# Kernel tuning notes

Hardware: AMD Instinct MI355X
Metric: run time of the kernel (lower is better)

## Reference

```python
import jax, jax.numpy as jnp
import numpy as np

EPS = 1e-12  # torch F.normalize default eps


def setup_inputs() -> dict:
    key = jax.random.key(0)
    k1, k2, k3, k4 = jax.random.split(key, 4)
    B, M, D = 4, 8192, 512
    N, P = 128, 1
    x = jax.random.normal(k1, (B, M, D), dtype=jnp.float32)
    phi = jax.random.normal(k2, (D, N, P), dtype=jnp.float32) * (1.0 / D ** 0.5)
    scale = jnp.ones((1,), dtype=jnp.float32)
    W = jax.random.normal(k3, (N, D, D), dtype=jnp.float32) * (1.0 / D ** 0.5)
    b = jax.random.normal(k4, (N, D), dtype=jnp.float32) * 0.01
    return {"x": x, "phi": phi, "scale": scale, "W": W, "b": b}


def _l2norm(v, axis):
    return v / jnp.maximum(jnp.linalg.norm(v, axis=axis, keepdims=True), EPS)


def reference(x, phi, scale, W, b):
    # normalize tokens along feature dim, phi along dim axis, scale phi
    xn = _l2norm(x, axis=2)                      # [B,M,D]
    phin = scale * _l2norm(phi, axis=0)          # [D,N,P]
    logits = jnp.einsum('bmd,dnp->bmnp', xn, phin)
    B, M, N, P = logits.shape
    d = jax.nn.softmax(logits, axis=1)           # dispatch weights (over tokens)
    c = jax.nn.softmax(logits.reshape(B, M, N * P), axis=-1).reshape(B, M, N, P)  # combine (over slots)
    xs = jnp.einsum('bmd,bmnp->bnpd', xn, d)     # slot inputs [B,N,P,D]
    # per-expert Linear, batched over experts (grouped GEMM)
    ys = jnp.einsum('bnpd,nde->bnpe', xs, W) + b[None, :, None, :]
    y = jnp.einsum('bnpd,bmnp->bmd', ys, c)
    return y
```

## Files before the change

kernel.cpp:

```cpp
#include <hip/hip_runtime.h>
#include <math.h>

#define B_ 4
#define M_ 8192
#define D_ 512
#define N_ 128
#define TOK (B_ * M_)
#define MC_ 16
#define MLEN (M_ / MC_)

#define OFF_CS 0
#define OFF_XS (OFF_CS + 512)
#define OFF_PBT (OFF_XS + B_ * N_ * D_)
#define OFF_E (OFF_PBT + N_ * D_ / 2)
#define OFF_EWT (OFF_E + (size_t)TOK * N_)
#define OFF_XBT (OFF_EWT + (size_t)N_ * TOK / 2)
#define OFF_YST (OFF_XBT + (size_t)D_ * TOK / 2)
#define OFF_XP (OFF_YST + B_ * D_ * N_ / 2)

typedef __attribute__((ext_vector_type(8))) short s16x8;
typedef __attribute__((ext_vector_type(4))) float f32x4;

__device__ inline short f2bf(float f) {
    union { float f; unsigned u; } v;
    v.f = f;
    unsigned r = v.u + 0x7fffu + ((v.u >> 16) & 1u);
    return (short)(r >> 16);
}

__global__ __launch_bounds__(128) void k_phinorm(const float* __restrict__ phi,
                                                 const float* __restrict__ scale,
                                                 short* __restrict__ pbt) {
    __shared__ float sred[128];
    int n = blockIdx.x, tid = threadIdx.x;
    float ss = 0.f;
    for (int d = tid; d < D_; d += 128) {
        float v = phi[d * N_ + n];
        ss += v * v;
    }
    sred[tid] = ss;
    __syncthreads();
    for (int s = 64; s > 0; s >>= 1) {
        if (tid < s) sred[tid] += sred[tid + s];
        __syncthreads();
    }
    float sc = scale[0] / fmaxf(sqrtf(sred[0]), 1e-12f);
    for (int d = tid; d < D_; d += 128) pbt[n * D_ + d] = f2bf(phi[d * N_ + n] * sc);
}

__global__ __launch_bounds__(512) void k_logits(const float* __restrict__ x,
                                                const short* __restrict__ pbt,
                                                float* __restrict__ E,
                                                short* __restrict__ ewt,
                                                short* __restrict__ xbt,
                                                float* __restrict__ colsum) {
    __shared__ short smem[2 * 128 * 40];
    __shared__ float rnS[128];
    short* As = smem;
    short* Bs = smem + 128 * 40;
    int t = threadIdx.x;
    int r0 = blockIdx.x * 128;
    int sm = t >> 2;
    int kq = (t & 3) * 8;
    const float* xrow = &x[(size_t)(r0 + sm) * D_ + kq];
    const short* brow = &pbt[sm * D_ + kq];
    int wid = t >> 6, lane = t & 63;
    int quad = lane >> 4, l15 = lane & 15;
    int mw = (wid >> 1) * 32, nw = (wid & 1) * 64;
    int dl = t & 31, mg = t >> 5;
    f32x4 acc[2][4] = {};
    float ss = 0.f;

    for (int k0 = 0; k0 < D_; k0 += 32) {
        float4 a0 = *(const float4*)&xrow[k0];
        float4 a1 = *(const float4*)&xrow[k0 + 4];
        ss += a0.x * a0.x + a0.y * a0.y + a0.z * a0.z + a0.w * a0.w +
              a1.x * a1.x + a1.y * a1.y + a1.z * a1.z + a1.w * a1.w;
        s16x8 av;
        av[0] = f2bf(a0.x); av[1] = f2bf(a0.y); av[2] = f2bf(a0.z); av[3] = f2bf(a0.w);
        av[4] = f2bf(a1.x); av[5] = f2bf(a1.y); av[6] = f2bf(a1.z); av[7] = f2bf(a1.w);
        s16x8 bv = *(const s16x8*)&brow[k0];
        *(s16x8*)&As[sm * 40 + kq] = av;
        *(s16x8*)&Bs[sm * 40 + kq] = bv;
        __syncthreads();
        s16x8 af[2], bf[4];
#pragma unroll
        for (int i = 0; i < 2; i++)
            af[i] = *(const s16x8*)&As[(mw + i * 16 + l15) * 40 + quad * 8];
#pragma unroll
        for (int j = 0; j < 4; j++)
            bf[j] = *(const s16x8*)&Bs[(nw + j * 16 + l15) * 40 + quad * 8];
#pragma unroll
        for (int i = 0; i < 2; i++)
#pragma unroll
            for (int j = 0; j < 4; j++)
                acc[i][j] = __builtin_amdgcn_mfma_f32_16x16x32_bf16(af[i], bf[j], acc[i][j], 0, 0, 0);
        {
            s16x8 tv;
#pragma unroll
            for (int r = 0; r < 8; r++) tv[r] = As[(mg * 8 + r) * 40 + dl];
            *(s16x8*)&xbt[(size_t)(k0 + dl) * TOK + r0 + mg * 8] = tv;
        }
        __syncthreads();
    }
    ss += __shfl_xor(ss, 1, 64);
    ss += __shfl_xor(ss, 2, 64);
    if ((t & 3) == 0) rnS[sm] = 1.0f / fmaxf(sqrtf(ss), 1e-12f);
    __syncthreads();

    int bb = r0 >> 13;
    float rv[2][4];
#pragma unroll
    for (int i = 0; i < 2; i++) {
        int ml = mw + i * 16 + quad * 4;
        rv[i][0] = rnS[ml]; rv[i][1] = rnS[ml + 1];
        rv[i][2] = rnS[ml + 2]; rv[i][3] = rnS[ml + 3];
    }
    short4 ebf[2][4];
#pragma unroll
    for (int j = 0; j < 4; j++) {
        int n = nw + j * 16 + l15;
        float cs = 0.f;
#pragma unroll
        for (int i = 0; i < 2; i++) {
            int mb = r0 + mw + i * 16 + quad * 4;
            f32x4 vv = acc[i][j];
            float e0 = __expf(vv[0] * rv[i][0]), e1 = __expf(vv[1] * rv[i][1]);
            float e2 = __expf(vv[2] * rv[i][2]), e3 = __expf(vv[3] * rv[i][3]);
            cs += e0 + e1 + e2 + e3;
            E[(size_t)(mb + 0) * N_ + n] = e0;
            E[(size_t)(mb + 1) * N_ + n] = e1;
            E[(size_t)(mb + 2) * N_ + n] = e2;
            E[(size_t)(mb + 3) * N_ + n] = e3;
            short4 eb = {f2bf(e0 * rv[i][0]), f2bf(e1 * rv[i][1]),
                         f2bf(e2 * rv[i][2]), f2bf(e3 * rv[i][3])};
            ebf[i][j] = eb;
        }
        cs += __shfl_xor(cs, 16, 64);
        cs += __shfl_xor(cs, 32, 64);
        if (lane < 16) atomicAdd(&colsum[bb * N_ + n], cs);
    }
    short* T = smem;
#pragma unroll
    for (int h = 0; h < 2; h++) {
        if ((wid & 1) == h) {
#pragma unroll
            for (int i = 0; i < 2; i++) {
                int mb = mw + i * 16 + quad * 4;
#pragma unroll
                for (int j = 0; j < 4; j++) {
                    int nl = j * 16 + l15;
                    *(short4*)&T[nl * 136 + mb] = ebf[i][j];
                }
            }
        }
        __syncthreads();
        {
            int nl = t >> 3, c = t & 7;
            s16x8 v0 = *(const s16x8*)&T[nl * 136 + c * 16];
            s16x8 v1 = *(const s16x8*)&T[nl * 136 + c * 16 + 8];
            size_t go = (size_t)(h * 64 + nl) * TOK + r0 + c * 16;
            *(s16x8*)&ewt[go] = v0;
            *(s16x8*)&ewt[go + 8] = v1;
        }
        __syncthreads();
    }
}

__global__ __launch_bounds__(256) void k_xs(const short* __restrict__ ewt,
                                            const short* __restrict__ xbt,
                                            float* __restrict__ part) {
    __shared__ short An[128 * 40];
    __shared__ short Bd[128 * 40];
    int t = threadIdx.x;
    int bid = blockIdx.x;
    int bi = (bid & 7) * 32 + (bid >> 3);
    int dt = bi & 3, mc = (bi >> 2) & 15, b = bi >> 6;
    int d0 = dt * 128;
    size_t mbase = (size_t)b * M_ + (size_t)mc * MLEN;
    int srow = t >> 1, shalf = (t & 1) * 16;
    const short* arow = &ewt[(size_t)srow * TOK + mbase + shalf];
    const short* brow = &xbt[(size_t)(d0 + srow) * TOK + mbase + shalf];
    int wid = t >> 6, lane = t & 63;
    int quad = lane >> 4, l15 = lane & 15;
    int nw = (wid >> 1) * 64, dw = (wid & 1) * 64;
    f32x4 acc[4][4] = {};

    for (int k0 = 0; k0 < MLEN; k0 += 32) {
        s16x8 a0 = *(const s16x8*)&arow[k0];
        s16x8 a1 = *(const s16x8*)&arow[k0 + 8];
        s16x8 b0 = *(const s16x8*)&brow[k0];
        s16x8 b1 = *(const s16x8*)&brow[k0 + 8];
        *(s16x8*)&An[srow * 40 + shalf] = a0;
        *(s16x8*)&An[srow * 40 + shalf + 8] = a1;
        *(s16x8*)&Bd[srow * 40 + shalf] = b0;
        *(s16x8*)&Bd[srow * 40 + shalf + 8] = b1;
        __syncthreads();
        s16x8 af[4], bf[4];
#pragma unroll
        for (int i = 0; i < 4; i++)
            af[i] = *(const s16x8*)&An[(nw + i * 16 + l15) * 40 + quad * 8];
#pragma unroll
        for (int j = 0; j < 4; j++)
            bf[j] = *(const s16x8*)&Bd[(dw + j * 16 + l15) * 40 + quad * 8];
#pragma unroll
        for (int i = 0; i < 4; i++)
#pragma unroll
            for (int j = 0; j < 4; j++)
                acc[i][j] = __builtin_amdgcn_mfma_f32_16x16x32_bf16(af[i], bf[j], acc[i][j], 0, 0, 0);
        __syncthreads();
    }
    size_t pbase = (((size_t)mc * B_ + b) * N_) * D_ + d0;
#pragma unroll
    for (int i = 0; i < 4; i++) {
        int nb = nw + i * 16 + quad * 4;
#pragma unroll
        for (int j = 0; j < 4; j++) {
            int d = dw + j * 16 + l15;
            f32x4 vv = acc[i][j];
            part[pbase + (size_t)(nb + 0) * D_ + d] = vv[0];
            part[pbase + (size_t)(nb + 1) * D_ + d] = vv[1];
            part[pbase + (size_t)(nb + 2) * D_ + d] = vv[2];
            part[pbase + (size_t)(nb + 3) * D_ + d] = vv[3];
        }
    }
}

__global__ __launch_bounds__(256) void k_xsum(const float* __restrict__ part,
                                              const float* __restrict__ colsum,
                                              float* __restrict__ xs) {
    int bi = blockIdx.x;
    int tid = threadIdx.x;
    float inv = 1.0f / colsum[bi];
    size_t base = (size_t)bi * D_ + tid * 2;
    float sx = 0.f, sy = 0.f;
#pragma unroll 8
    for (int mc = 0; mc < MC_; mc++) {
        float2 v = *(const float2*)&part[(size_t)mc * (B_ * N_ * D_) + base];
        sx += v.x;
        sy += v.y;
    }
    float2 o = {sx * inv, sy * inv};
    *(float2*)&xs[base] = o;
}

__global__ __launch_bounds__(256) void k_ys(const float* __restrict__ xs,
                                            const float* __restrict__ W,
                                            const float* __restrict__ bias,
                                            short* __restrict__ ysT) {
    __shared__ float xsn[B_][D_];
    int bi = blockIdx.x;
    int n = bi >> 2, eq = bi & 3;
    int tid = threadIdx.x;
    {
        int lb = tid >> 6, ld = (tid & 63) * 4;
        *(float4*)&xsn[lb][ld] = *(const float4*)&xs[((size_t)lb * N_ + n) * D_ + ld];
        *(float4*)&xsn[lb][256 + ld] =
            *(const float4*)&xs[((size_t)lb * N_ + n) * D_ + 256 + ld];
    }
    __syncthreads();
    int b = tid >> 6;
    int e = eq * 128 + (tid & 63) * 2;
    const float* Wn = W + (size_t)n * D_ * D_ + e;
    float a0 = 0.f, a1 = 0.f;
#pragma unroll 8
    for (int d = 0; d < D_; d++) {
        float2 w = *(const float2*)&Wn[(size_t)d * D_];
        float xv = xsn[b][d];
        a0 += xv * w.x;
        a1 += xv * w.y;
    }
    float2 bv = *(const float2*)&bias[n * D_ + e];
    ysT[((size_t)b * D_ + e) * N_ + n] = f2bf(a0 + bv.x);
    ysT[((size_t)b * D_ + e + 1) * N_ + n] = f2bf(a1 + bv.y);
}

__global__ __launch_bounds__(256) void k_combine(const float* __restrict__ E,
                                                 const short* __restrict__ ysT,
                                                 float* __restrict__ y) {
    __shared__ short As[128 * 40];
    __shared__ short Bs[128 * 40];
    __shared__ float rsA[2][128];
    __shared__ float rsinv[128];
    int t = threadIdx.x;
    int bid = blockIdx.x;
    int bi = (bid & 7) * 128 + (bid >> 3);
    int dt = bi & 3, mt = bi >> 2;
    int r0 = mt * 128, d0 = dt * 128;
    int bb = r0 >> 13;
    int sm = t >> 1, nh = (t & 1) * 16;
    const float* erow = &E[(size_t)(r0 + sm) * N_ + nh];
    const short* yrow = &ysT[((size_t)bb * D_ + d0 + sm) * N_ + nh];
    int wid = t >> 6, lane = t & 63;
    int quad = lane >> 4, l15 = lane & 15;
    int mw = (wid >> 1) * 64, dw = (wid & 1) * 64;
    f32x4 acc[4][4] = {};
    float rsp = 0.f;

    for (int ks = 0; ks < 4; ks++) {
        int n0 = ks * 32;
        float4 e0 = *(const float4*)&erow[n0];
        float4 e1 = *(const float4*)&erow[n0 + 4];
        float4 e2 = *(const float4*)&erow[n0 + 8];
        float4 e3 = *(const float4*)&erow[n0 + 12];
        rsp += e0.x + e0.y + e0.z + e0.w + e1.x + e1.y + e1.z + e1.w +
               e2.x + e2.y + e2.z + e2.w + e3.x + e3.y + e3.z + e3.w;
        short4 w0 = {f2bf(e0.x), f2bf(e0.y), f2bf(e0.z), f2bf(e0.w)};
        short4 w1 = {f2bf(e1.x), f2bf(e1.y), f2bf(e1.z), f2bf(e1.w)};
        short4 w2 = {f2bf(e2.x), f2bf(e2.y), f2bf(e2.z), f2bf(e2.w)};
        short4 w3 = {f2bf(e3.x), f2bf(e3.y), f2bf(e3.z), f2bf(e3.w)};
        *(short4*)&As[sm * 40 + nh + 0] = w0;
        *(short4*)&As[sm * 40 + nh + 4] = w1;
        *(short4*)&As[sm * 40 + nh + 8] = w2;
        *(short4*)&As[sm * 40 + nh + 12] = w3;
        *(s16x8*)&Bs[sm * 40 + nh] = *(const s16x8*)&yrow[n0];
        *(s16x8*)&Bs[sm * 40 + nh + 8] = *(const s16x8*)&yrow[n0 + 8];
        __syncthreads();
        s16x8 af[4], bf[4];
#pragma unroll
        for (int i = 0; i < 4; i++)
            af[i] = *(const s16x8*)&As[(mw + i * 16 + l15) * 40 + quad * 8];
#pragma unroll
        for (int j = 0; j < 4; j++)
            bf[j] = *(const s16x8*)&Bs[(dw + j * 16 + l15) * 40 + quad * 8];
#pragma unroll
        for (int i = 0; i < 4; i++)
#pragma unroll
            for (int j = 0; j < 4; j++)
                acc[i][j] = __builtin_amdgcn_mfma_f32_16x16x32_bf16(af[i], bf[j], acc[i][j], 0, 0, 0);
        __syncthreads();
    }
    rsA[t & 1][sm] = rsp;
    __syncthreads();
    if (t < 128) rsinv[t] = 1.0f / (rsA[0][t] + rsA[1][t]);
    __syncthreads();
#pragma unroll
    for (int i = 0; i < 4; i++) {
        int mb = mw + i * 16 + quad * 4;
        float i0 = rsinv[mb], i1 = rsinv[mb + 1], i2 = rsinv[mb + 2], i3 = rsinv[mb + 3];
#pragma unroll
        for (int j = 0; j < 4; j++) {
            int d = d0 + dw + j * 16 + l15;
            f32x4 v = acc[i][j];
            y[(size_t)(r0 + mb + 0) * D_ + d] = v[0] * i0;
            y[(size_t)(r0 + mb + 1) * D_ + d] = v[1] * i1;
            y[(size_t)(r0 + mb + 2) * D_ + d] = v[2] * i2;
            y[(size_t)(r0 + mb + 3) * D_ + d] = v[3] * i3;
        }
    }
}

extern "C" void kernel_launch(void* const* d_in, const int* in_sizes, int n_in,
                              void* d_out, int out_size, void* d_ws, size_t ws_size,
                              hipStream_t stream) {
    const float* x = (const float*)d_in[0];
    const float* phi = (const float*)d_in[1];
    const float* scale = (const float*)d_in[2];
    const float* W = (const float*)d_in[3];
    const float* bias = (const float*)d_in[4];
    float* y = (float*)d_out;
    float* ws = (float*)d_ws;

    float* colsum = ws + OFF_CS;
    float* xs = ws + OFF_XS;
    short* pbt = (short*)(ws + OFF_PBT);
    float* E = ws + OFF_E;
    short* ewt = (short*)(ws + OFF_EWT);
    short* xbt = (short*)(ws + OFF_XBT);
    short* ysT = (short*)(ws + OFF_YST);
    float* part = ws + OFF_XP;

    hipMemsetAsync(colsum, 0, 512 * sizeof(float), stream);

    k_phinorm<<<N_, 128, 0, stream>>>(phi, scale, pbt);
    k_logits<<<TOK / 128, 512, 0, stream>>>(x, pbt, E, ewt, xbt, colsum);
    k_xs<<<B_ * MC_ * 4, 256, 0, stream>>>(ewt, xbt, part);
    k_xsum<<<B_ * N_, 256, 0, stream>>>(part, colsum, xs);
    k_ys<<<N_ * 4, 256, 0, stream>>>(xs, W, bias, ysT);
    k_combine<<<(TOK / 128) * 4, 256, 0, stream>>>(E, ysT, y);
}
```

Baseline: 327.1 us.

## Fuse slot-input GEMM into logits kernel with sliced atomic accumulation

New measurement: 422.8 us. 1.29x slower.

```diff
diff --git a/kernel.cpp b/kernel.cpp
--- a/kernel.cpp
+++ b/kernel.cpp
@@ -6,17 +6,13 @@
 #define D_ 512
 #define N_ 128
 #define TOK (B_ * M_)
-#define MC_ 16
-#define MLEN (M_ / MC_)
+#define NSL 8
 
 #define OFF_CS 0
-#define OFF_XS (OFF_CS + 512)
-#define OFF_PBT (OFF_XS + B_ * N_ * D_)
+#define OFF_XSA 512
+#define OFF_PBT (OFF_XSA + NSL * B_ * N_ * D_)
 #define OFF_E (OFF_PBT + N_ * D_ / 2)
-#define OFF_EWT (OFF_E + (size_t)TOK * N_)
-#define OFF_XBT (OFF_EWT + (size_t)N_ * TOK / 2)
-#define OFF_YST (OFF_XBT + (size_t)D_ * TOK / 2)
-#define OFF_XP (OFF_YST + B_ * D_ * N_ / 2)
+#define OFF_YST (OFF_E + (size_t)TOK * N_)
 
 typedef __attribute__((ext_vector_type(8))) short s16x8;
 typedef __attribute__((ext_vector_type(4))) float f32x4;
@@ -48,30 +44,34 @@
     for (int d = tid; d < D_; d += 128) pbt[n * D_ + d] = f2bf(phi[d * N_ + n] * sc);
 }
 
-__global__ __launch_bounds__(512) void k_logits(const float* __restrict__ x,
+__global__ __launch_bounds__(256) void k_logits(const float* __restrict__ x,
                                                 const short* __restrict__ pbt,
                                                 float* __restrict__ E,
-                                                short* __restrict__ ewt,
-                                                short* __restrict__ xbt,
-                                                float* __restrict__ colsum) {
-    __shared__ short smem[2 * 128 * 40];
-    __shared__ float rnS[128];
+                                                float* __restrict__ colsum,
+                                                float* __restrict__ xsa) {
+    __shared__ short smem[64 * 40 + 128 * 40];
+    __shared__ float rnS[64];
     short* As = smem;
-    short* Bs = smem + 128 * 40;
+    short* Bs = smem + 64 * 40;
+    short* T = smem;
+
     int t = threadIdx.x;
-    int r0 = blockIdx.x * 128;
-    int sm = t >> 2;
-    int kq = (t & 3) * 8;
-    const float* xrow = &x[(size_t)(r0 + sm) * D_ + kq];
-    const short* brow = &pbt[sm * D_ + kq];
+    int r0 = blockIdx.x * 64;
+    int slice = blockIdx.x & 7;
+    int sma = t >> 2, kqa = (t & 3) * 8;
+    int smb = t >> 1, khb = (t & 1) * 16;
+    const float* xrow = &x[(size_t)(r0 + sma) * D_ + kqa];
+    const short* brow = &pbt[smb * D_ + khb];
     int wid = t >> 6, lane = t & 63;
     int quad = lane >> 4, l15 = lane & 15;
-    int mw = (wid >> 1) * 32, nw = (wid & 1) * 64;
-    int dl = t & 31, mg = t >> 5;
-    f32x4 acc[2][4] = {};
+    int mw = wid * 16;
+    f32x4 acc[8] = {};
+    s16x8 bf2[8][2];
     float ss = 0.f;
 
-    for (int k0 = 0; k0 < D_; k0 += 32) {
+#pragma unroll
+    for (int kt = 0; kt < 16; kt++) {
+        int k0 = kt * 32;
         float4 a0 = *(const float4*)&xrow[k0];
         float4 a1 = *(const float4*)&xrow[k0 + 4];
         ss += a0.x * a0.x + a0.y * a0.y + a0.z * a0.z + a0.w * a0.w +
@@ -79,172 +79,107 @@
         s16x8 av;
         av[0] = f2bf(a0.x); av[1] = f2bf(a0.y); av[2] = f2bf(a0.z); av[3] = f2bf(a0.w);
         av[4] = f2bf(a1.x); av[5] = f2bf(a1.y); av[6] = f2bf(a1.z); av[7] = f2bf(a1.w);
-        s16x8 bv = *(const s16x8*)&brow[k0];
-        *(s16x8*)&As[sm * 40 + kq] = av;
-        *(s16x8*)&Bs[sm * 40 + kq] = bv;
-        __syncthreads();
-        s16x8 af[2], bf[4];
-#pragma unroll
-        for (int i = 0; i < 2; i++)
-            af[i] = *(const s16x8*)&As[(mw + i * 16 + l15) * 40 + quad * 8];
-#pragma unroll
-        for (int j = 0; j < 4; j++)
-            bf[j] = *(const s16x8*)&Bs[(nw + j * 16 + l15) * 40 + quad * 8];
-#pragma unroll
-        for (int i = 0; i < 2; i++)
-#pragma unroll
-            for (int j = 0; j < 4; j++)
-                acc[i][j] = __builtin_amdgcn_mfma_f32_16x16x32_bf16(af[i], bf[j], acc[i][j], 0, 0, 0);
-        {
-            s16x8 tv;
-#pragma unroll
-            for (int r = 0; r < 8; r++) tv[r] = As[(mg * 8 + r) * 40 + dl];
-            *(s16x8*)&xbt[(size_t)(k0 + dl) * TOK + r0 + mg * 8] = tv;
+        s16x8 bv0 = *(const s16x8*)&brow[k0];
+        s16x8 bv1 = *(const s16x8*)&brow[k0 + 8];
+        *(s16x8*)&As[sma * 40 + kqa] = av;
+        *(s16x8*)&Bs[smb * 40 + khb] = bv0;
+        *(s16x8*)&Bs[smb * 40 + khb + 8] = bv1;
+        __syncthreads();
+        s16x8 af = *(const s16x8*)&As[(mw + l15) * 40 + quad * 8];
+        s16x8 bfr[8];
+#pragma unroll
+        for (int j = 0; j < 8; j++)
+            bfr[j] = *(const s16x8*)&Bs[(j * 16 + l15) * 40 + quad * 8];
+#pragma unroll
+        for (int j = 0; j < 8; j++)
+            acc[j] = __builtin_amdgcn_mfma_f32_16x16x32_bf16(af, bfr[j], acc[j], 0, 0, 0);
+        if ((kt >> 2) == wid) {
+#pragma unroll
+            for (int djl = 0; djl < 2; djl++)
+#pragma unroll
+                for (int mk = 0; mk < 2; mk++) {
+                    s16x8 tv;
+#pragma unroll
+                    for (int jj = 0; jj < 8; jj++)
+                        tv[jj] = As[(mk * 32 + quad * 8 + jj) * 40 + djl * 16 + l15];
+                    bf2[(kt & 3) * 2 + djl][mk] = tv;
+                }
         }
         __syncthreads();
     }
     ss += __shfl_xor(ss, 1, 64);
     ss += __shfl_xor(ss, 2, 64);
-    if ((t & 3) == 0) rnS[sm] = 1.0f / fmaxf(sqrtf(ss), 1e-12f);
+    if ((t & 3) == 0) rnS[sma] = 1.0f / fmaxf(sqrtf(ss), 1e-12f);
     __syncthreads();
 
     int bb = r0 >> 13;
-    float rv[2][4];
-#pragma unroll
-    for (int i = 0; i < 2; i++) {
-        int ml = mw + i * 16 + quad * 4;
-        rv[i][0] = rnS[ml]; rv[i][1] = rnS[ml + 1];
-        rv[i][2] = rnS[ml + 2]; rv[i][3] = rnS[ml + 3];
-    }
-    short4 ebf[2][4];
-#pragma unroll
-    for (int j = 0; j < 4; j++) {
-        int n = nw + j * 16 + l15;
-        float cs = 0.f;
-#pragma unroll
-        for (int i = 0; i < 2; i++) {
-            int mb = r0 + mw + i * 16 + quad * 4;
-            f32x4 vv = acc[i][j];
-            float e0 = __expf(vv[0] * rv[i][0]), e1 = __expf(vv[1] * rv[i][1]);
-            float e2 = __expf(vv[2] * rv[i][2]), e3 = __expf(vv[3] * rv[i][3]);
-            cs += e0 + e1 + e2 + e3;
-            E[(size_t)(mb + 0) * N_ + n] = e0;
-            E[(size_t)(mb + 1) * N_ + n] = e1;
-            E[(size_t)(mb + 2) * N_ + n] = e2;
-            E[(size_t)(mb + 3) * N_ + n] = e3;
-            short4 eb = {f2bf(e0 * rv[i][0]), f2bf(e1 * rv[i][1]),
-                         f2bf(e2 * rv[i][2]), f2bf(e3 * rv[i][3])};
-            ebf[i][j] = eb;
-        }
+    float rv0 = rnS[mw + quad * 4 + 0], rv1 = rnS[mw + quad * 4 + 1];
+    float rv2 = rnS[mw + quad * 4 + 2], rv3 = rnS[mw + quad * 4 + 3];
+    short4 ebf[8];
+#pragma unroll
+    for (int j = 0; j < 8; j++) {
+        int n = j * 16 + l15;
+        int mb = r0 + mw + quad * 4;
+        f32x4 vv = acc[j];
+        float e0 = __expf(vv[0] * rv0), e1 = __expf(vv[1] * rv1);
+        float e2 = __expf(vv[2] * rv2), e3 = __expf(vv[3] * rv3);
+        float cs = e0 + e1 + e2 + e3;
+        E[(size_t)(mb + 0) * N_ + n] = e0;
+        E[(size_t)(mb + 1) * N_ + n] = e1;
+        E[(size_t)(mb + 2) * N_ + n] = e2;
+        E[(size_t)(mb + 3) * N_ + n] = e3;
+        short4 eb = {f2bf(e0 * rv0), f2bf(e1 * rv1), f2bf(e2 * rv2), f2bf(e3 * rv3)};
+        ebf[j] = eb;
         cs += __shfl_xor(cs, 16, 64);
         cs += __shfl_xor(cs, 32, 64);
-        if (lane < 16) atomicAdd(&colsum[bb * N_ + n], cs);
-    }
-    short* T = smem;
+        if (lane < 16) unsafeAtomicAdd(&colsum[bb * N_ + n], cs);
+    }
+
+    size_t xbase = (size_t)slice * (B_ * N_ * D_) + (size_t)bb * (N_ * D_);
+    int dstrip = wid * 128;
 #pragma unroll
     for (int h = 0; h < 2; h++) {
-        if ((wid & 1) == h) {
-#pragma unroll
-            for (int i = 0; i < 2; i++) {
-                int mb = mw + i * 16 + quad * 4;
-#pragma unroll
-                for (int j = 0; j < 4; j++) {
-                    int nl = j * 16 + l15;
-                    *(short4*)&T[nl * 136 + mb] = ebf[i][j];
+        __syncthreads();
+#pragma unroll
+        for (int j = 0; j < 4; j++) {
+            int nl = j * 16 + l15;
+            *(short4*)&T[nl * 72 + mw + quad * 4] = ebf[h * 4 + j];
+        }
+        __syncthreads();
+#pragma unroll
+        for (int p = 0; p < 2; p++) {
+            f32x4 c2[4][4] = {};
+#pragma unroll
+            for (int mk = 0; mk < 2; mk++) {
+                s16x8 af2[4];
+#pragma unroll
+                for (int nb = 0; nb < 4; nb++)
+                    af2[nb] = *(const s16x8*)&T[(nb * 16 + l15) * 72 + mk * 32 + quad * 8];
+#pragma unroll
+                for (int nb = 0; nb < 4; nb++)
+#pragma unroll
+                    for (int jj = 0; jj < 4; jj++)
+                        c2[nb][jj] = __builtin_amdgcn_mfma_f32_16x16x32_bf16(
+                            af2[nb], bf2[p * 4 + jj][mk], c2[nb][jj], 0, 0, 0);
+            }
+#pragma unroll
+            for (int nb = 0; nb < 4; nb++) {
+                int n = h * 64 + nb * 16 + quad * 4;
+#pragma unroll
+                for (int jj = 0; jj < 4; jj++) {
+                    int d = dstrip + p * 64 + jj * 16 + l15;
+#pragma unroll
+                    for (int rr = 0; rr < 4; rr++)
+                        unsafeAtomicAdd(&xsa[xbase + (size_t)(n + rr) * D_ + d],
+                                        c2[nb][jj][rr]);
                 }
             }
         }
-        __syncthreads();
-        {
-            int nl = t >> 3, c = t & 7;
-            s16x8 v0 = *(const s16x8*)&T[nl * 136 + c * 16];
-            s16x8 v1 = *(const s16x8*)&T[nl * 136 + c * 16 + 8];
-            size_t go = (size_t)(h * 64 + nl) * TOK + r0 + c * 16;
-            *(s16x8*)&ewt[go] = v0;
-            *(s16x8*)&ewt[go + 8] = v1;
-        }
-        __syncthreads();
-    }
-}
-
-__global__ __launch_bounds__(256) void k_xs(const short* __restrict__ ewt,
-                                            const short* __restrict__ xbt,
-                                            float* __restrict__ part) {
-    __shared__ short An[128 * 40];
-    __shared__ short Bd[128 * 40];
-    int t = threadIdx.x;
-    int bid = blockIdx.x;
-    int bi = (bid & 7) * 32 + (bid >> 3);
-    int dt = bi & 3, mc = (bi >> 2) & 15, b = bi >> 6;
-    int d0 = dt * 128;
-    size_t mbase = (size_t)b * M_ + (size_t)mc * MLEN;
-    int srow = t >> 1, shalf = (t & 1) * 16;
-    const short* arow = &ewt[(size_t)srow * TOK + mbase + shalf];
-    const short* brow = &xbt[(size_t)(d0 + srow) * TOK + mbase + shalf];
-    int wid = t >> 6, lane = t & 63;
-    int quad = lane >> 4, l15 = lane & 15;
-    int nw = (wid >> 1) * 64, dw = (wid & 1) * 64;
-    f32x4 acc[4][4] = {};
-
-    for (int k0 = 0; k0 < MLEN; k0 += 32) {
-        s16x8 a0 = *(const s16x8*)&arow[k0];
-        s16x8 a1 = *(const s16x8*)&arow[k0 + 8];
-        s16x8 b0 = *(const s16x8*)&brow[k0];
-        s16x8 b1 = *(const s16x8*)&brow[k0 + 8];
-        *(s16x8*)&An[srow * 40 + shalf] = a0;
-        *(s16x8*)&An[srow * 40 + shalf + 8] = a1;
-        *(s16x8*)&Bd[srow * 40 + shalf] = b0;
-        *(s16x8*)&Bd[srow * 40 + shalf + 8] = b1;
-        __syncthreads();
-        s16x8 af[4], bf[4];
-#pragma unroll
-        for (int i = 0; i < 4; i++)
-            af[i] = *(const s16x8*)&An[(nw + i * 16 + l15) * 40 + quad * 8];
-#pragma unroll
-        for (int j = 0; j < 4; j++)
-            bf[j] = *(const s16x8*)&Bd[(dw + j * 16 + l15) * 40 + quad * 8];
-#pragma unroll
-        for (int i = 0; i < 4; i++)
-#pragma unroll
-            for (int j = 0; j < 4; j++)
-                acc[i][j] = __builtin_amdgcn_mfma_f32_16x16x32_bf16(af[i], bf[j], acc[i][j], 0, 0, 0);
-        __syncthreads();
-    }
-    size_t pbase = (((size_t)mc * B_ + b) * N_) * D_ + d0;
-#pragma unroll
-    for (int i = 0; i < 4; i++) {
-        int nb = nw + i * 16 + quad * 4;
-#pragma unroll
-        for (int j = 0; j < 4; j++) {
-            int d = dw + j * 16 + l15;
-            f32x4 vv = acc[i][j];
-            part[pbase + (size_t)(nb + 0) * D_ + d] = vv[0];
-            part[pbase + (size_t)(nb + 1) * D_ + d] = vv[1];
-            part[pbase + (size_t)(nb + 2) * D_ + d] = vv[2];
-            part[pbase + (size_t)(nb + 3) * D_ + d] = vv[3];
-        }
-    }
-}
-
-__global__ __launch_bounds__(256) void k_xsum(const float* __restrict__ part,
-                                              const float* __restrict__ colsum,
-                                              float* __restrict__ xs) {
-    int bi = blockIdx.x;
-    int tid = threadIdx.x;
-    float inv = 1.0f / colsum[bi];
-    size_t base = (size_t)bi * D_ + tid * 2;
-    float sx = 0.f, sy = 0.f;
-#pragma unroll 8
-    for (int mc = 0; mc < MC_; mc++) {
-        float2 v = *(const float2*)&part[(size_t)mc * (B_ * N_ * D_) + base];
-        sx += v.x;
-        sy += v.y;
-    }
-    float2 o = {sx * inv, sy * inv};
-    *(float2*)&xs[base] = o;
-}
-
-__global__ __launch_bounds__(256) void k_ys(const float* __restrict__ xs,
+    }
+}
+
+__global__ __launch_bounds__(256) void k_ys(const float* __restrict__ xsa,
+                                            const float* __restrict__ colsum,
                                             const float* __restrict__ W,
                                             const float* __restrict__ bias,
                                             short* __restrict__ ysT) {
@@ -253,10 +188,22 @@
     int n = bi >> 2, eq = bi & 3;
     int tid = threadIdx.x;
     {
-        int lb = tid >> 6, ld = (tid & 63) * 4;
-        *(float4*)&xsn[lb][ld] = *(const float4*)&xs[((size_t)lb * N_ + n) * D_ + ld];
-        *(float4*)&xsn[lb][256 + ld] =
-            *(const float4*)&xs[((size_t)lb * N_ + n) * D_ + 256 + ld];
+        int lb = tid >> 6, ld = (tid & 63) * 8;
+        float inv = 1.0f / colsum[lb * N_ + n];
+        size_t base = ((size_t)lb * N_ + n) * D_ + ld;
+        float s0 = 0, s1 = 0, s2 = 0, s3 = 0, s4 = 0, s5 = 0, s6 = 0, s7 = 0;
+#pragma unroll
+        for (int s = 0; s < NSL; s++) {
+            const float* p = &xsa[(size_t)s * (B_ * N_ * D_) + base];
+            float4 v0 = *(const float4*)p;
+            float4 v1 = *(const float4*)(p + 4);
+            s0 += v0.x; s1 += v0.y; s2 += v0.z; s3 += v0.w;
+            s4 += v1.x; s5 += v1.y; s6 += v1.z; s7 += v1.w;
+        }
+        float4 o0 = {s0 * inv, s1 * inv, s2 * inv, s3 * inv};
+        float4 o1 = {s4 * inv, s5 * inv, s6 * inv, s7 * inv};
+        *(float4*)&xsn[lb][ld] = o0;
+        *(float4*)&xsn[lb][ld + 4] = o1;
     }
     __syncthreads();
     int b = tid >> 6;
@@ -362,20 +309,15 @@
     float* ws = (float*)d_ws;
 
     float* colsum = ws + OFF_CS;
-    float* xs = ws + OFF_XS;
+    float* xsa = ws + OFF_XSA;
     short* pbt = (short*)(ws + OFF_PBT);
     float* E = ws + OFF_E;
-    short* ewt = (short*)(ws + OFF_EWT);
-    short* xbt = (short*)(ws + OFF_XBT);
     short* ysT = (short*)(ws + OFF_YST);
-    float* part = ws + OFF_XP;
-
-    hipMemsetAsync(colsum, 0, 512 * sizeof(float), stream);
+
+    hipMemsetAsync(colsum, 0, (size_t)(512 + NSL * B_ * N_ * D_) * sizeof(float), stream);
 
     k_phinorm<<<N_, 128, 0, stream>>>(phi, scale, pbt);
-    k_logits<<<TOK / 128, 512, 0, stream>>>(x, pbt, E, ewt, xbt, colsum);
-    k_xs<<<B_ * MC_ * 4, 256, 0, stream>>>(ewt, xbt, part);
-    k_xsum<<<B_ * N_, 256, 0, stream>>>(part, colsum, xs);
-    k_ys<<<N_ * 4, 256, 0, stream>>>(xs, W, bias, ysT);
+    k_logits<<<TOK / 64, 256, 0, stream>>>(x, pbt, E, colsum, xsa);
+    k_ys<<<N_ * 4, 256, 0, stream>>>(xsa, colsum, W, bias, ysT);
     k_combine<<<(TOK / 128) * 4, 256, 0, stream>>>(E, ysT, y);
 }
```

## Double-buffer LDS in logits and xs GEMMs, fold partial reduction into ys

Applied to the files above, without the earlier changes.

Measured after the change: 325.9 us. Within noise of the previous version (-0.4%).

```diff
diff --git a/kernel.cpp b/kernel.cpp
--- a/kernel.cpp
+++ b/kernel.cpp
@@ -10,13 +10,12 @@
 #define MLEN (M_ / MC_)
 
 #define OFF_CS 0
-#define OFF_XS (OFF_CS + 512)
-#define OFF_PBT (OFF_XS + B_ * N_ * D_)
+#define OFF_PBT (OFF_CS + 512)
 #define OFF_E (OFF_PBT + N_ * D_ / 2)
-#define OFF_EWT (OFF_E + (size_t)TOK * N_)
-#define OFF_XBT (OFF_EWT + (size_t)N_ * TOK / 2)
-#define OFF_YST (OFF_XBT + (size_t)D_ * TOK / 2)
-#define OFF_XP (OFF_YST + B_ * D_ * N_ / 2)
+#define OFF_YST (OFF_E + (size_t)TOK * N_)
+#define OFF_XBT (OFF_YST + B_ * D_ * N_ / 2)
+#define OFF_EWT (OFF_XBT + (size_t)D_ * TOK / 2)
+#define OFF_XP (OFF_EWT + (size_t)N_ * TOK / 2)
 
 typedef __attribute__((ext_vector_type(8))) short s16x8;
 typedef __attribute__((ext_vector_type(4))) float f32x4;
@@ -54,10 +53,11 @@
                                                 short* __restrict__ ewt,
                                                 short* __restrict__ xbt,
                                                 float* __restrict__ colsum) {
-    __shared__ short smem[2 * 128 * 40];
+    __shared__ short As[2][128 * 40];
+    __shared__ short Bs[2][128 * 40];
     __shared__ float rnS[128];
-    short* As = smem;
-    short* Bs = smem + 128 * 40;
+    short* T = &As[0][0];
+
     int t = threadIdx.x;
     int r0 = blockIdx.x * 128;
     int sm = t >> 2;
@@ -71,35 +71,56 @@
     f32x4 acc[2][4] = {};
     float ss = 0.f;
 
-    for (int k0 = 0; k0 < D_; k0 += 32) {
-        float4 a0 = *(const float4*)&xrow[k0];
-        float4 a1 = *(const float4*)&xrow[k0 + 4];
+    {
+        float4 a0 = *(const float4*)&xrow[0];
+        float4 a1 = *(const float4*)&xrow[4];
+        s16x8 bv = *(const s16x8*)&brow[0];
         ss += a0.x * a0.x + a0.y * a0.y + a0.z * a0.z + a0.w * a0.w +
               a1.x * a1.x + a1.y * a1.y + a1.z * a1.z + a1.w * a1.w;
         s16x8 av;
         av[0] = f2bf(a0.x); av[1] = f2bf(a0.y); av[2] = f2bf(a0.z); av[3] = f2bf(a0.w);
         av[4] = f2bf(a1.x); av[5] = f2bf(a1.y); av[6] = f2bf(a1.z); av[7] = f2bf(a1.w);
-        s16x8 bv = *(const s16x8*)&brow[k0];
-        *(s16x8*)&As[sm * 40 + kq] = av;
-        *(s16x8*)&Bs[sm * 40 + kq] = bv;
-        __syncthreads();
-        s16x8 af[2], bf[4];
+        *(s16x8*)&As[0][sm * 40 + kq] = av;
+        *(s16x8*)&Bs[0][sm * 40 + kq] = bv;
+    }
+    __syncthreads();
+
+#pragma unroll
+    for (int kt = 0; kt < 16; kt++) {
+        int cur = kt & 1;
+        float4 na0, na1;
+        s16x8 nbv;
+        if (kt < 15) {
+            na0 = *(const float4*)&xrow[(kt + 1) * 32];
+            na1 = *(const float4*)&xrow[(kt + 1) * 32 + 4];
+            nbv = *(const s16x8*)&brow[(kt + 1) * 32];
+        }
+        s16x8 af[2], bfr[4];
 #pragma unroll
         for (int i = 0; i < 2; i++)
-            af[i] = *(const s16x8*)&As[(mw + i * 16 + l15) * 40 + quad * 8];
+            af[i] = *(const s16x8*)&As[cur][(mw + i * 16 + l15) * 40 + quad * 8];
 #pragma unroll
         for (int j = 0; j < 4; j++)
-            bf[j] = *(const s16x8*)&Bs[(nw + j * 16 + l15) * 40 + quad * 8];
+            bfr[j] = *(const s16x8*)&Bs[cur][(nw + j * 16 + l15) * 40 + quad * 8];
 #pragma unroll
         for (int i = 0; i < 2; i++)
 #pragma unroll
             for (int j = 0; j < 4; j++)
-                acc[i][j] = __builtin_amdgcn_mfma_f32_16x16x32_bf16(af[i], bf[j], acc[i][j], 0, 0, 0);
+                acc[i][j] = __builtin_amdgcn_mfma_f32_16x16x32_bf16(af[i], bfr[j], acc[i][j], 0, 0, 0);
         {
             s16x8 tv;
 #pragma unroll
-            for (int r = 0; r < 8; r++) tv[r] = As[(mg * 8 + r) * 40 + dl];
-            *(s16x8*)&xbt[(size_t)(k0 + dl) * TOK + r0 + mg * 8] = tv;
+            for (int r = 0; r < 8; r++) tv[r] = As[cur][(mg * 8 + r) * 40 + dl];
+            *(s16x8*)&xbt[(size_t)(kt * 32 + dl) * TOK + r0 + mg * 8] = tv;
+        }
+        if (kt < 15) {
+            ss += na0.x * na0.x + na0.y * na0.y + na0.z * na0.z + na0.w * na0.w +
+                  na1.x * na1.x + na1.y * na1.y + na1.z * na1.z + na1.w * na1.w;
+            s16x8 nav;
+            nav[0] = f2bf(na0.x); nav[1] = f2bf(na0.y); nav[2] = f2bf(na0.z); nav[3] = f2bf(na0.w);
+            nav[4] = f2bf(na1.x); nav[5] = f2bf(na1.y); nav[6] = f2bf(na1.z); nav[7] = f2bf(na1.w);
+            *(s16x8*)&As[cur ^ 1][sm * 40 + kq] = nav;
+            *(s16x8*)&Bs[cur ^ 1][sm * 40 + kq] = nbv;
         }
         __syncthreads();
     }
@@ -140,7 +161,6 @@
         cs += __shfl_xor(cs, 32, 64);
         if (lane < 16) atomicAdd(&colsum[bb * N_ + n], cs);
     }
-    short* T = smem;
 #pragma unroll
     for (int h = 0; h < 2; h++) {
         if ((wid & 1) == h) {
@@ -167,47 +187,57 @@
     }
 }
 
-__global__ __launch_bounds__(256) void k_xs(const short* __restrict__ ewt,
+__global__ __launch_bounds__(512) void k_xs(const short* __restrict__ ewt,
                                             const short* __restrict__ xbt,
                                             float* __restrict__ part) {
-    __shared__ short An[128 * 40];
-    __shared__ short Bd[128 * 40];
+    __shared__ short An[2][128 * 40];
+    __shared__ short Bd[2][128 * 40];
     int t = threadIdx.x;
     int bid = blockIdx.x;
     int bi = (bid & 7) * 32 + (bid >> 3);
     int dt = bi & 3, mc = (bi >> 2) & 15, b = bi >> 6;
     int d0 = dt * 128;
     size_t mbase = (size_t)b * M_ + (size_t)mc * MLEN;
-    int srow = t >> 1, shalf = (t & 1) * 16;
-    const short* arow = &ewt[(size_t)srow * TOK + mbase + shalf];
-    const short* brow = &xbt[(size_t)(d0 + srow) * TOK + mbase + shalf];
+    int rs = t >> 2, kq = (t & 3) * 8;
+    const short* arow = &ewt[(size_t)rs * TOK + mbase + kq];
+    const short* brow = &xbt[(size_t)(d0 + rs) * TOK + mbase + kq];
     int wid = t >> 6, lane = t & 63;
     int quad = lane >> 4, l15 = lane & 15;
-    int nw = (wid >> 1) * 64, dw = (wid & 1) * 64;
-    f32x4 acc[4][4] = {};
-
-    for (int k0 = 0; k0 < MLEN; k0 += 32) {
-        s16x8 a0 = *(const s16x8*)&arow[k0];
-        s16x8 a1 = *(const s16x8*)&arow[k0 + 8];
-        s16x8 b0 = *(const s16x8*)&brow[k0];
-        s16x8 b1 = *(const s16x8*)&brow[k0 + 8];
-        *(s16x8*)&An[srow * 40 + shalf] = a0;
-        *(s16x8*)&An[srow * 40 + shalf + 8] = a1;
-        *(s16x8*)&Bd[srow * 40 + shalf] = b0;
-        *(s16x8*)&Bd[srow * 40 + shalf + 8] = b1;
-        __syncthreads();
-        s16x8 af[4], bf[4];
+    int nw = (wid >> 2) * 64, dw = (wid & 3) * 32;
+    f32x4 acc[4][2] = {};
+
+    {
+        s16x8 ra = *(const s16x8*)&arow[0];
+        s16x8 rb = *(const s16x8*)&brow[0];
+        *(s16x8*)&An[0][rs * 40 + kq] = ra;
+        *(s16x8*)&Bd[0][rs * 40 + kq] = rb;
+    }
+    __syncthreads();
+
+#pragma unroll
+    for (int kt = 0; kt < 16; kt++) {
+        int cur = kt & 1;
+        s16x8 ra, rb;
+        if (kt < 15) {
+            ra = *(const s16x8*)&arow[(kt + 1) * 32];
+            rb = *(const s16x8*)&brow[(kt + 1) * 32];
+        }
+        s16x8 af[4], bf[2];
 #pragma unroll
         for (int i = 0; i < 4; i++)
-            af[i] = *(const s16x8*)&An[(nw + i * 16 + l15) * 40 + quad * 8];
-#pragma unroll
-        for (int j = 0; j < 4; j++)
-            bf[j] = *(const s16x8*)&Bd[(dw + j * 16 + l15) * 40 + quad * 8];
+            af[i] = *(const s16x8*)&An[cur][(nw + i * 16 + l15) * 40 + quad * 8];
+#pragma unroll
+        for (int j = 0; j < 2; j++)
+            bf[j] = *(const s16x8*)&Bd[cur][(dw + j * 16 + l15) * 40 + quad * 8];
 #pragma unroll
         for (int i = 0; i < 4; i++)
 #pragma unroll
-            for (int j = 0; j < 4; j++)
+            for (int j = 0; j < 2; j++)
                 acc[i][j] = __builtin_amdgcn_mfma_f32_16x16x32_bf16(af[i], bf[j], acc[i][j], 0, 0, 0);
+        if (kt < 15) {
+            *(s16x8*)&An[cur ^ 1][rs * 40 + kq] = ra;
+            *(s16x8*)&Bd[cur ^ 1][rs * 40 + kq] = rb;
+        }
         __syncthreads();
     }
     size_t pbase = (((size_t)mc * B_ + b) * N_) * D_ + d0;
@@ -215,7 +245,7 @@
     for (int i = 0; i < 4; i++) {
         int nb = nw + i * 16 + quad * 4;
 #pragma unroll
-        for (int j = 0; j < 4; j++) {
+        for (int j = 0; j < 2; j++) {
             int d = dw + j * 16 + l15;
             f32x4 vv = acc[i][j];
             part[pbase + (size_t)(nb + 0) * D_ + d] = vv[0];
@@ -226,25 +256,8 @@
     }
 }
 
-__global__ __launch_bounds__(256) void k_xsum(const float* __restrict__ part,
-                                              const float* __restrict__ colsum,
-                                              float* __restrict__ xs) {
-    int bi = blockIdx.x;
-    int tid = threadIdx.x;
-    float inv = 1.0f / colsum[bi];
-    size_t base = (size_t)bi * D_ + tid * 2;
-    float sx = 0.f, sy = 0.f;
-#pragma unroll 8
-    for (int mc = 0; mc < MC_; mc++) {
-        float2 v = *(const float2*)&part[(size_t)mc * (B_ * N_ * D_) + base];
-        sx += v.x;
-        sy += v.y;
-    }
-    float2 o = {sx * inv, sy * inv};
-    *(float2*)&xs[base] = o;
-}
-
-__global__ __launch_bounds__(256) void k_ys(const float* __restrict__ xs,
+__global__ __launch_bounds__(256) void k_ys(const float* __restrict__ part,
+                                            const float* __restrict__ colsum,
                                             const float* __restrict__ W,
                                             const float* __restrict__ bias,
                                             short* __restrict__ ysT) {
@@ -253,10 +266,21 @@
     int n = bi >> 2, eq = bi & 3;
     int tid = threadIdx.x;
     {
-        int lb = tid >> 6, ld = (tid & 63) * 4;
-        *(float4*)&xsn[lb][ld] = *(const float4*)&xs[((size_t)lb * N_ + n) * D_ + ld];
-        *(float4*)&xsn[lb][256 + ld] =
-            *(const float4*)&xs[((size_t)lb * N_ + n) * D_ + 256 + ld];
+        int lb = tid >> 6, ld = (tid & 63) * 8;
+        float inv = 1.0f / colsum[lb * N_ + n];
+        float s0 = 0, s1 = 0, s2 = 0, s3 = 0, s4 = 0, s5 = 0, s6 = 0, s7 = 0;
+#pragma unroll
+        for (int mc = 0; mc < MC_; mc++) {
+            const float* p = &part[(((size_t)mc * B_ + lb) * N_ + n) * D_ + ld];
+            float4 v0 = *(const float4*)p;
+            float4 v1 = *(const float4*)(p + 4);
+            s0 += v0.x; s1 += v0.y; s2 += v0.z; s3 += v0.w;
+            s4 += v1.x; s5 += v1.y; s6 += v1.z; s7 += v1.w;
+        }
+        float4 o0 = {s0 * inv, s1 * inv, s2 * inv, s3 * inv};
+        float4 o1 = {s4 * inv, s5 * inv, s6 * inv, s7 * inv};
+        *(float4*)&xsn[lb][ld] = o0;
+        *(float4*)&xsn[lb][ld + 4] = o1;
     }
     __syncthreads();
     int b = tid >> 6;
@@ -362,20 +386,18 @@
     float* ws = (float*)d_ws;
 
     float* colsum = ws + OFF_CS;
-    float* xs = ws + OFF_XS;
     short* pbt = (short*)(ws + OFF_PBT);
     float* E = ws + OFF_E;
+    short* ysT = (short*)(ws + OFF_YST);
+    short* xbt = (short*)(ws + OFF_XBT);
     short* ewt = (short*)(ws + OFF_EWT);
-    short* xbt = (short*)(ws + OFF_XBT);
-    short* ysT = (short*)(ws + OFF_YST);
     float* part = ws + OFF_XP;
 
     hipMemsetAsync(colsum, 0, 512 * sizeof(float), stream);
 
     k_phinorm<<<N_, 128, 0, stream>>>(phi, scale, pbt);
     k_logits<<<TOK / 128, 512, 0, stream>>>(x, pbt, E, ewt, xbt, colsum);
-    k_xs<<<B_ * MC_ * 4, 256, 0, stream>>>(ewt, xbt, part);
-    k_xsum<<<B_ * N_, 256, 0, stream>>>(part, colsum, xs);
-    k_ys<<<N_ * 4, 256, 0, stream>>>(xs, W, bias, ysT);
+    k_xs<<<B_ * MC_ * 4, 512, 0, stream>>>(ewt, xbt, part);
+    k_ys<<<N_ * 4, 256, 0, stream>>>(part, colsum, W, bias, ysT);
     k_combine<<<(TOK / 128) * 4, 256, 0, stream>>>(E, ysT, y);
 }
```
